# Kernel optimization log

Measured on AMD Instinct MI355X. Metric: run time of the kernel, lower is better.

Reference implementation:

```python
import jax, jax.numpy as jnp
import numpy as np
from jax import lax

B, L, F = 32, 2048, 76   # batch, seq_len, feat_dim
H = 128                  # conv hidden channels
D = 128                  # prototype dim (last 1x1 conv)
P = 128                  # number of prototypes
CLASS_SIZE = 2


def setup_inputs() -> dict:
    key = jax.random.key(0)
    ks = jax.random.split(key, 8)
    w = lambda k, shape: jax.random.normal(k, shape, jnp.float32) * 0.05
    return {
        "x": jax.random.normal(ks[0], (B, L, F), jnp.float32),
        "W1": w(ks[1], (H, F, 5)), "b1": jnp.zeros((H,), jnp.float32),
        "W2": w(ks[2], (H, H, 5)), "b2": jnp.zeros((H,), jnp.float32),
        "W3": w(ks[3], (H, H, 5)), "b3": jnp.zeros((H,), jnp.float32),
        "Wo1": w(ks[4], (D, H)), "bo1": jnp.zeros((D,), jnp.float32),
        "Wo2": w(ks[5], (D, D)), "bo2": jnp.zeros((D,), jnp.float32),
        "prototypes": jax.random.uniform(ks[6], (P, D), jnp.float32),
        "protop_classes": jnp.concatenate([jnp.zeros(P // 2, jnp.int32), jnp.ones(P // 2, jnp.int32)]),
    }


def _conv1d_same(h, W, b):
    # h: (B, C, L), W: (O, C, K=5), symmetric padding 2 == torch padding=k//2
    y = lax.conv_general_dilated(h, W, window_strides=(1,), padding=[(2, 2)],
                                 dimension_numbers=("NCW", "OIW", "NCW"))
    return y + b[None, :, None]


def _maxpool2(h):
    return lax.reduce_window(h, -jnp.inf, lax.max, (1, 1, 2), (1, 1, 2), "VALID")


def reference(x, W1, b1, W2, b2, W3, b3, Wo1, bo1, Wo2, bo2, prototypes, protop_classes):
    h = jnp.transpose(x, (0, 2, 1))  # (B, F, L)
    for W, b in ((W1, b1), (W2, b2), (W3, b3)):
        h = _maxpool2(jax.nn.relu(_conv1d_same(h, W, b)))
    # 1x1 convs as channel matmuls
    h = jax.nn.relu(jnp.einsum("bcl,oc->bol", h, Wo1) + bo1[None, :, None])
    h = jax.nn.relu(jnp.einsum("bcl,oc->bol", h, Wo2) + bo2[None, :, None])
    f = jnp.transpose(h, (0, 2, 1))  # (B, Lp=256, D)
    # l2_conv via ||a-b||^2 = ||a||^2 - 2 a.b + ||b||^2 (same math, GEMM form)
    d2 = (jnp.sum(f * f, axis=-1, keepdims=True)
          - 2.0 * jnp.einsum("bld,pd->blp", f, prototypes)
          + jnp.sum(prototypes * prototypes, axis=-1))  # (B, Lp, P)
    dis = jnp.sqrt(jnp.maximum(d2, 1e-12))
    min_dis = jnp.min(dis, axis=1)  # (B, P): min over patches
    # dis2sim, 'log' activation
    sim = jnp.log((min_dis + 1.0) / (min_dis + 1e-4))
    # init_weights: last_layer.weight[i,j] = 1 if protop_classes[j]==i else -0.5
    lw = jnp.where(protop_classes[None, :] == jnp.arange(CLASS_SIZE)[:, None], 1.0, -0.5)
    out = jax.nn.sigmoid(sim @ lw.T)  # (B, CLASS_SIZE)
    return out, min_dis
```

## Files before the change

kernel.cpp:

```cpp
#include <hip/hip_runtime.h>
#include <cmath>


typedef __attribute__((ext_vector_type(8))) short short8;
typedef __attribute__((ext_vector_type(4))) float f32x4;

__device__ __forceinline__ unsigned short f2bf(float v) {
    union { float f; unsigned u; } x; x.f = v;
    unsigned r = x.u + 0x7fffu + ((x.u >> 16) & 1u);
    return (unsigned short)(r >> 16);
}
__device__ __forceinline__ float bf2f(unsigned short b) {
    union { unsigned u; float f; } x; x.u = ((unsigned)b) << 16;
    return x.f;
}

__device__ void pack_conv_w(int t, int total, const float* __restrict__ W, int C,
                            unsigned short* __restrict__ dst)
{
    if (t >= total) return;
    int lane = t & 63, rest = t >> 6;
    int mf = rest & 7; rest >>= 3;
    int kk = rest % 5, cc = rest / 5;
    int m = mf * 16 + (lane & 15);
    int cb = cc * 32 + (lane >> 4) * 8;
    unsigned short v[8];
#pragma unroll
    for (int j = 0; j < 8; ++j) {
        int c = cb + j;
        v[j] = (c < C) ? f2bf(W[((size_t)m * C + c) * 5 + kk]) : (unsigned short)0;
    }
    *(uint4*)&dst[(size_t)t * 8] = *(uint4*)v;
}

__device__ void pack_mat(int t, const float* __restrict__ M, unsigned short* __restrict__ dst)
{
    if (t >= 2048) return;
    int lane = t & 63, mf = (t >> 6) & 7, cc = t >> 9;
    int m = mf * 16 + (lane & 15);
    int c0 = cc * 32 + (lane >> 4) * 8;
    unsigned short v[8];
#pragma unroll
    for (int j = 0; j < 8; ++j) v[j] = f2bf(M[(size_t)m * 128 + c0 + j]);
    *(uint4*)&dst[(size_t)t * 8] = *(uint4*)v;
}

__global__ __launch_bounds__(256)
void prep_weights_kernel(const float* __restrict__ W1, const float* __restrict__ W2,
                         const float* __restrict__ W3, const float* __restrict__ Wo1,
                         const float* __restrict__ Wo2, const float* __restrict__ protos,
                         unsigned short* A1, unsigned short* A2, unsigned short* A3,
                         unsigned short* AW1, unsigned short* AW2, unsigned short* AP,
                         float* pn, unsigned* pm_bits)
{
    int t = blockIdx.x * 256 + threadIdx.x;
    switch (blockIdx.y) {
    case 0: pack_conv_w(t, 7680,  W1, 76,  A1); break;
    case 1: pack_conv_w(t, 10240, W2, 128, A2); break;
    case 2: pack_conv_w(t, 10240, W3, 128, A3); break;
    case 3: pack_mat(t, Wo1, AW1); break;
    case 4: pack_mat(t, Wo2, AW2); break;
    case 5: pack_mat(t, protos, AP); break;
    case 6:
        if (t < 128) {
            float s = 0.f;
            for (int d = 0; d < 128; ++d) {
                float v = bf2f(f2bf(protos[(size_t)t * 128 + d]));
                s = fmaf(v, v, s);
            }
            pn[t] = s;
        }
        break;
    case 7:
        if (t < 4096) pm_bits[t] = 0x7F800000u;
        break;
    }
}

__global__ __launch_bounds__(256)
void conv1_mfma(const float* __restrict__ x, const unsigned short* __restrict__ Af,
                const float* __restrict__ bias, unsigned short* __restrict__ out)
{
    constexpr int LIN = 2048, LOUT = 1024, CPL = 104;
    __shared__ __align__(16) unsigned short s_in[68 * CPL];
    __shared__ float s_bias[128];

    const int tid = threadIdx.x;
    const int b   = blockIdx.y;
    const int l0  = blockIdx.x * 64;

    if (tid < 128) s_bias[tid] = bias[tid];

    for (int idx = tid; idx < 68 * 24; idx += 256) {
        int pos = idx / 24, c0 = (idx % 24) * 4;
        int l = l0 - 2 + pos;
        unsigned short v[4] = {0, 0, 0, 0};
        if (c0 < 76 && l >= 0 && l < LIN) {
            float4 xv = *(const float4*)&x[((size_t)b * LIN + l) * 76 + c0];
            v[0] = f2bf(xv.x); v[1] = f2bf(xv.y); v[2] = f2bf(xv.z); v[3] = f2bf(xv.w);
        }
        *(uint2*)&s_in[pos * CPL + c0] = *(uint2*)v;
    }
    __syncthreads();

    const int lane = tid & 63;
    const int mf0  = (tid >> 6) * 2;
    const int lc   = lane & 15;
    const int lk   = (lane >> 4) * 8;

    const f32x4 zero = {0.f, 0.f, 0.f, 0.f};
    f32x4 acc[2][4];
#pragma unroll
    for (int i = 0; i < 2; ++i)
#pragma unroll
        for (int j = 0; j < 4; ++j) acc[i][j] = zero;

    for (int cc = 0; cc < 3; ++cc) {
#pragma unroll
        for (int kk = 0; kk < 5; ++kk) {
            const int step = cc * 5 + kk;
            short8 a[2];
#pragma unroll
            for (int i = 0; i < 2; ++i)
                a[i] = *(const short8*)&Af[(((size_t)step * 8 + mf0 + i) * 64 + lane) * 8];
            short8 bb[4];
#pragma unroll
            for (int j = 0; j < 4; ++j)
                bb[j] = *(const short8*)&s_in[(j * 16 + lc + kk) * CPL + cc * 32 + lk];
#pragma unroll
            for (int i = 0; i < 2; ++i)
#pragma unroll
                for (int j = 0; j < 4; ++j)
                    acc[i][j] = __builtin_amdgcn_mfma_f32_16x16x32_bf16(a[i], bb[j], acc[i][j], 0, 0, 0);
        }
    }

    const int lp0 = l0 >> 1;
#pragma unroll
    for (int i = 0; i < 2; ++i) {
        const int ch0 = (mf0 + i) * 16 + (lane >> 4) * 4;
#pragma unroll
        for (int j = 0; j < 4; ++j) {
            const int n = j * 16 + lc;
            unsigned short pk[4];
#pragma unroll
            for (int r = 0; r < 4; ++r) {
                float v = fmaxf(acc[i][j][r] + s_bias[ch0 + r], 0.f);
                float o = __shfl_xor(v, 1);
                pk[r] = f2bf(fmaxf(v, o));
            }
            if ((lc & 1) == 0)
                *(uint2*)&out[((size_t)b * LOUT + lp0 + (n >> 1)) * 128 + ch0] = *(uint2*)pk;
        }
    }
}

__global__ __launch_bounds__(256)
void conv2_mfma(const unsigned short* __restrict__ in, const unsigned short* __restrict__ Af,
                const float* __restrict__ bias, unsigned short* __restrict__ out)
{
    constexpr int LIN = 1024, LOUT = 512, CPL = 136;
    __shared__ __align__(16) unsigned short s_in[68 * CPL];
    __shared__ float s_bias[128];

    const int tid = threadIdx.x;
    const int b   = blockIdx.y;
    const int l0  = blockIdx.x * 64;

    if (tid < 128) s_bias[tid] = bias[tid];

    for (int idx = tid; idx < 68 * 16; idx += 256) {
        int pos = idx >> 4, co = (idx & 15) * 8;
        int l = l0 - 2 + pos;
        uint4 v = make_uint4(0u, 0u, 0u, 0u);
        if (l >= 0 && l < LIN)
            v = *(const uint4*)&in[((size_t)b * LIN + l) * 128 + co];
        *(uint4*)&s_in[pos * CPL + co] = v;
    }
    __syncthreads();

    const int lane = tid & 63;
    const int mf0  = (tid >> 6) * 2;
    const int lc   = lane & 15;
    const int lk   = (lane >> 4) * 8;

    const f32x4 zero = {0.f, 0.f, 0.f, 0.f};
    f32x4 acc[2][4];
#pragma unroll
    for (int i = 0; i < 2; ++i)
#pragma unroll
        for (int j = 0; j < 4; ++j) acc[i][j] = zero;

    for (int cc = 0; cc < 4; ++cc) {
#pragma unroll
        for (int kk = 0; kk < 5; ++kk) {
            const int step = cc * 5 + kk;
            short8 a[2];
#pragma unroll
            for (int i = 0; i < 2; ++i)
                a[i] = *(const short8*)&Af[(((size_t)step * 8 + mf0 + i) * 64 + lane) * 8];
            short8 bb[4];
#pragma unroll
            for (int j = 0; j < 4; ++j)
                bb[j] = *(const short8*)&s_in[(j * 16 + lc + kk) * CPL + cc * 32 + lk];
#pragma unroll
            for (int i = 0; i < 2; ++i)
#pragma unroll
                for (int j = 0; j < 4; ++j)
                    acc[i][j] = __builtin_amdgcn_mfma_f32_16x16x32_bf16(a[i], bb[j], acc[i][j], 0, 0, 0);
        }
    }

    const int lp0 = l0 >> 1;
#pragma unroll
    for (int i = 0; i < 2; ++i) {
        const int ch0 = (mf0 + i) * 16 + (lane >> 4) * 4;
#pragma unroll
        for (int j = 0; j < 4; ++j) {
            const int n = j * 16 + lc;
            unsigned short pk[4];
#pragma unroll
            for (int r = 0; r < 4; ++r) {
                float v = fmaxf(acc[i][j][r] + s_bias[ch0 + r], 0.f);
                float o = __shfl_xor(v, 1);
                pk[r] = f2bf(fmaxf(v, o));
            }
            if ((lc & 1) == 0)
                *(uint2*)&out[((size_t)b * LOUT + lp0 + (n >> 1)) * 128 + ch0] = *(uint2*)pk;
        }
    }
}

__global__ __launch_bounds__(256)
void conv3_head(const unsigned short* __restrict__ in, const unsigned short* __restrict__ Af,
                const float* __restrict__ bias,
                const unsigned short* __restrict__ AW1, const float* __restrict__ bo1,
                const unsigned short* __restrict__ AW2, const float* __restrict__ bo2,
                const unsigned short* __restrict__ AP,  const float* __restrict__ pn,
                unsigned* __restrict__ pm_bits)
{
    constexpr int LIN = 512, CPL = 136, CP = 136;
    __shared__ __align__(16) unsigned short s_in[68 * CPL];
    __shared__ __align__(16) unsigned short s_f[32 * CP];
    __shared__ float s_bias[128];
    __shared__ float s_part[4 * 32];
    __shared__ float s_fn[32];

    const int tid = threadIdx.x;
    const int b   = blockIdx.y;
    const int l0  = blockIdx.x * 64;

    if (tid < 128) s_bias[tid] = bias[tid];

    for (int idx = tid; idx < 68 * 16; idx += 256) {
        int pos = idx >> 4, co = (idx & 15) * 8;
        int l = l0 - 2 + pos;
        uint4 v = make_uint4(0u, 0u, 0u, 0u);
        if (l >= 0 && l < LIN)
            v = *(const uint4*)&in[((size_t)b * LIN + l) * 128 + co];
        *(uint4*)&s_in[pos * CPL + co] = v;
    }
    __syncthreads();

    const int lane = tid & 63;
    const int mf0  = (tid >> 6) * 2;
    const int lc   = lane & 15;
    const int lk   = (lane >> 4) * 8;

    const f32x4 zero = {0.f, 0.f, 0.f, 0.f};

    f32x4 acc[2][4];
#pragma unroll
    for (int i = 0; i < 2; ++i)
#pragma unroll
        for (int j = 0; j < 4; ++j) acc[i][j] = zero;

    for (int cc = 0; cc < 4; ++cc) {
#pragma unroll
        for (int kk = 0; kk < 5; ++kk) {
            const int step = cc * 5 + kk;
            short8 a[2];
#pragma unroll
            for (int i = 0; i < 2; ++i)
                a[i] = *(const short8*)&Af[(((size_t)step * 8 + mf0 + i) * 64 + lane) * 8];
            short8 bb[4];
#pragma unroll
            for (int j = 0; j < 4; ++j)
                bb[j] = *(const short8*)&s_in[(j * 16 + lc + kk) * CPL + cc * 32 + lk];
#pragma unroll
            for (int i = 0; i < 2; ++i)
#pragma unroll
                for (int j = 0; j < 4; ++j)
                    acc[i][j] = __builtin_amdgcn_mfma_f32_16x16x32_bf16(a[i], bb[j], acc[i][j], 0, 0, 0);
        }
    }

#pragma unroll
    for (int i = 0; i < 2; ++i) {
        const int ch0 = (mf0 + i) * 16 + (lane >> 4) * 4;
#pragma unroll
        for (int j = 0; j < 4; ++j) {
            const int n = j * 16 + lc;
            unsigned short pk[4];
#pragma unroll
            for (int r = 0; r < 4; ++r) {
                float v = fmaxf(acc[i][j][r] + s_bias[ch0 + r], 0.f);
                float o = __shfl_xor(v, 1);
                pk[r] = f2bf(fmaxf(v, o));
            }
            if ((lc & 1) == 0)
                *(uint2*)&s_f[(n >> 1) * CP + ch0] = *(uint2*)pk;
        }
    }
    __syncthreads();

    f32x4 hacc[2][2];

    auto gemm32 = [&](const unsigned short* __restrict__ A) {
#pragma unroll
        for (int i = 0; i < 2; ++i)
#pragma unroll
            for (int j = 0; j < 2; ++j) hacc[i][j] = zero;
        for (int cc = 0; cc < 4; ++cc) {
            short8 a[2];
#pragma unroll
            for (int i = 0; i < 2; ++i)
                a[i] = *(const short8*)&A[(((size_t)cc * 8 + mf0 + i) * 64 + lane) * 8];
            short8 bb[2];
#pragma unroll
            for (int j = 0; j < 2; ++j)
                bb[j] = *(const short8*)&s_f[(j * 16 + lc) * CP + cc * 32 + lk];
#pragma unroll
            for (int i = 0; i < 2; ++i)
#pragma unroll
                for (int j = 0; j < 2; ++j)
                    hacc[i][j] = __builtin_amdgcn_mfma_f32_16x16x32_bf16(a[i], bb[j], hacc[i][j], 0, 0, 0);
        }
    };

    auto store_relu32 = [&](const float* __restrict__ bv) {
        __syncthreads();
#pragma unroll
        for (int i = 0; i < 2; ++i) {
            const int ch0 = (mf0 + i) * 16 + (lane >> 4) * 4;
#pragma unroll
            for (int j = 0; j < 2; ++j) {
                const int n = j * 16 + lc;
                unsigned short pk[4];
#pragma unroll
                for (int r = 0; r < 4; ++r)
                    pk[r] = f2bf(fmaxf(hacc[i][j][r] + bv[ch0 + r], 0.f));
                *(uint2*)&s_f[n * CP + ch0] = *(uint2*)pk;
            }
        }
        __syncthreads();
    };

    gemm32(AW1); store_relu32(bo1);
    gemm32(AW2); store_relu32(bo2);

    if (tid < 128) {
        int n = tid >> 2, part = tid & 3;
        float s = 0.f;
        for (int c = part * 32; c < part * 32 + 32; ++c) {
            float v = bf2f(s_f[n * CP + c]);
            s = fmaf(v, v, s);
        }
        s_part[part * 32 + n] = s;
    }
    __syncthreads();
    if (tid < 32)
        s_fn[tid] = s_part[tid] + s_part[32 + tid] + s_part[64 + tid] + s_part[96 + tid];
    __syncthreads();

    gemm32(AP);

#pragma unroll
    for (int i = 0; i < 2; ++i) {
#pragma unroll
        for (int r = 0; r < 4; ++r) {
            const int p = (mf0 + i) * 16 + (lane >> 4) * 4 + r;
            float m = 3.0e38f;
#pragma unroll
            for (int j = 0; j < 2; ++j) {
                const int n = j * 16 + lc;
                float d2 = s_fn[n] + pn[p] - 2.f * hacc[i][j][r];
                m = fminf(m, sqrtf(fmaxf(d2, 1e-12f)));
            }
#pragma unroll
            for (int s = 1; s < 16; s <<= 1)
                m = fminf(m, __shfl_xor(m, s));
            if (lc == 0)
                atomicMin(&pm_bits[(size_t)b * 128 + p], __float_as_uint(m));
        }
    }
}

__global__ __launch_bounds__(128)
void finalize_kernel(const float* __restrict__ pm,
                     const int* __restrict__ classes,
                     float* __restrict__ out)
{
    __shared__ float r0[128], r1[128];
    const int b = blockIdx.x, p = threadIdx.x;
    float m = pm[(size_t)b * 128 + p];
    out[64 + b * 128 + p] = m;

    float sim = logf((m + 1.0f) / (m + 1e-4f));
    int cls = classes[p];
    r0[p] = (cls == 0) ? sim : -0.5f * sim;
    r1[p] = (cls == 1) ? sim : -0.5f * sim;
    __syncthreads();
    for (int s = 64; s > 0; s >>= 1) {
        if (p < s) { r0[p] += r0[p + s]; r1[p] += r1[p + s]; }
        __syncthreads();
    }
    if (p == 0) {
        out[b * 2 + 0] = 1.f / (1.f + expf(-r0[0]));
        out[b * 2 + 1] = 1.f / (1.f + expf(-r1[0]));
    }
}

extern "C" void kernel_launch(void* const* d_in, const int* in_sizes, int n_in,
                              void* d_out, int out_size, void* d_ws, size_t ws_size,
                              hipStream_t stream)
{
    (void)in_sizes; (void)n_in; (void)out_size; (void)ws_size;
    const float* x    = (const float*)d_in[0];
    const float* W1   = (const float*)d_in[1];
    const float* b1   = (const float*)d_in[2];
    const float* W2   = (const float*)d_in[3];
    const float* b2   = (const float*)d_in[4];
    const float* W3   = (const float*)d_in[5];
    const float* b3   = (const float*)d_in[6];
    const float* Wo1  = (const float*)d_in[7];
    const float* bo1  = (const float*)d_in[8];
    const float* Wo2  = (const float*)d_in[9];
    const float* bo2  = (const float*)d_in[10];
    const float* prot = (const float*)d_in[11];
    const int*   cls  = (const int*)d_in[12];
    float* out = (float*)d_out;

    char* ws = (char*)d_ws;
    unsigned short* h1 = (unsigned short*)(ws);
    unsigned short* h2 = (unsigned short*)(ws + 8388608);
    const size_t FR = 12582912;
    unsigned short* A1  = (unsigned short*)(ws + FR);
    unsigned short* A2  = (unsigned short*)(ws + FR + 122880);
    unsigned short* A3  = (unsigned short*)(ws + FR + 286720);
    unsigned short* AW1 = (unsigned short*)(ws + FR + 450560);
    unsigned short* AW2 = (unsigned short*)(ws + FR + 483328);
    unsigned short* AP  = (unsigned short*)(ws + FR + 516096);
    float*          pn  = (float*)(ws + FR + 548864);
    unsigned*       pm  = (unsigned*)(ws + FR + 549376);

    prep_weights_kernel<<<dim3(40, 8), 256, 0, stream>>>(W1, W2, W3, Wo1, Wo2, prot,
                                                         A1, A2, A3, AW1, AW2, AP, pn, pm);
    conv1_mfma<<<dim3(32, 32), 256, 0, stream>>>(x,  A1, b1, h1);
    conv2_mfma<<<dim3(16, 32), 256, 0, stream>>>(h1, A2, b2, h2);
    conv3_head<<<dim3(8, 32), 256, 0, stream>>>(h2, A3, b3, AW1, bo1, AW2, bo2, AP, pn, pm);
    finalize_kernel<<<32, 128, 0, stream>>>((const float*)pm, cls, out);
}
```

Before: 133.1 us.

## Fuse all three conv stages and head into one kernel with halo recompute

Replaces the separate conv1, conv2 and conv3+head kernels with one 512-thread kernel per (batch, 256-position tile). Each block loads an input tile with an 18-position halo, runs conv1 into shared memory, then conv2 and conv3 from shared memory, and finishes with the 1x1 head and prototype distances. This removes the global-memory round trips of the h1/h2 intermediates and two kernel launches. In exchange it recomputes halo columns, launches only 256 blocks, and needs large shared memory and many accumulator registers, which may limit occupancy.

```diff
diff --git a/kernel.cpp b/kernel.cpp
--- a/kernel.cpp
+++ b/kernel.cpp
@@ -77,45 +77,20 @@
     }
 }
 
-__global__ __launch_bounds__(256)
-void conv1_mfma(const float* __restrict__ x, const unsigned short* __restrict__ Af,
-                const float* __restrict__ bias, unsigned short* __restrict__ out)
-{
-    constexpr int LIN = 2048, LOUT = 1024, CPL = 104;
-    __shared__ __align__(16) unsigned short s_in[68 * CPL];
-    __shared__ float s_bias[128];
-
-    const int tid = threadIdx.x;
-    const int b   = blockIdx.y;
-    const int l0  = blockIdx.x * 64;
-
-    if (tid < 128) s_bias[tid] = bias[tid];
-
-    for (int idx = tid; idx < 68 * 24; idx += 256) {
-        int pos = idx / 24, c0 = (idx % 24) * 4;
-        int l = l0 - 2 + pos;
-        unsigned short v[4] = {0, 0, 0, 0};
-        if (c0 < 76 && l >= 0 && l < LIN) {
-            float4 xv = *(const float4*)&x[((size_t)b * LIN + l) * 76 + c0];
-            v[0] = f2bf(xv.x); v[1] = f2bf(xv.y); v[2] = f2bf(xv.z); v[3] = f2bf(xv.w);
-        }
-        *(uint2*)&s_in[pos * CPL + c0] = *(uint2*)v;
-    }
-    __syncthreads();
-
-    const int lane = tid & 63;
-    const int mf0  = (tid >> 6) * 2;
-    const int lc   = lane & 15;
-    const int lk   = (lane >> 4) * 8;
-
-    const f32x4 zero = {0.f, 0.f, 0.f, 0.f};
-    f32x4 acc[2][4];
+template <int NJ, int NCC, int STRIDE, int ROWOFF, int ROWMAX>
+__device__ __forceinline__ void conv_k(const unsigned short* __restrict__ Af,
+                                       const unsigned short* __restrict__ sIn,
+                                       int nbase, int mf0, int lane,
+                                       f32x4 (&acc)[2][NJ])
+{
+    const int lc = lane & 15;
+    const int lk = (lane >> 4) * 8;
 #pragma unroll
     for (int i = 0; i < 2; ++i)
 #pragma unroll
-        for (int j = 0; j < 4; ++j) acc[i][j] = zero;
-
-    for (int cc = 0; cc < 3; ++cc) {
+        for (int j = 0; j < NJ; ++j) acc[i][j] = (f32x4){0.f, 0.f, 0.f, 0.f};
+
+    for (int cc = 0; cc < NCC; ++cc) {
 #pragma unroll
         for (int kk = 0; kk < 5; ++kk) {
             const int step = cc * 5 + kk;
@@ -123,247 +98,208 @@
 #pragma unroll
             for (int i = 0; i < 2; ++i)
                 a[i] = *(const short8*)&Af[(((size_t)step * 8 + mf0 + i) * 64 + lane) * 8];
-            short8 bb[4];
-#pragma unroll
-            for (int j = 0; j < 4; ++j)
-                bb[j] = *(const short8*)&s_in[(j * 16 + lc + kk) * CPL + cc * 32 + lk];
-#pragma unroll
-            for (int i = 0; i < 2; ++i)
-#pragma unroll
-                for (int j = 0; j < 4; ++j)
+            short8 bb[NJ];
+#pragma unroll
+            for (int j = 0; j < NJ; ++j) {
+                int row = nbase + j * 16 + lc + kk + ROWOFF;
+                if (ROWMAX >= 0) row = min(max(row, 0), ROWMAX);
+                bb[j] = *(const short8*)&sIn[row * STRIDE + cc * 32 + lk];
+            }
+#pragma unroll
+            for (int j = 0; j < NJ; ++j)
+#pragma unroll
+                for (int i = 0; i < 2; ++i)
                     acc[i][j] = __builtin_amdgcn_mfma_f32_16x16x32_bf16(a[i], bb[j], acc[i][j], 0, 0, 0);
         }
     }
-
-    const int lp0 = l0 >> 1;
+}
+
+__device__ __forceinline__ void gemm_head(const unsigned short* __restrict__ Af,
+                                          const unsigned short* __restrict__ s_f,
+                                          int nbase, int mf0, int lane,
+                                          f32x4 (&acc)[2])
+{
+    const int lc = lane & 15;
+    const int lk = (lane >> 4) * 8;
+    acc[0] = (f32x4){0.f, 0.f, 0.f, 0.f};
+    acc[1] = (f32x4){0.f, 0.f, 0.f, 0.f};
+#pragma unroll
+    for (int cc = 0; cc < 4; ++cc) {
+        short8 a[2];
+#pragma unroll
+        for (int i = 0; i < 2; ++i)
+            a[i] = *(const short8*)&Af[(((size_t)cc * 8 + mf0 + i) * 64 + lane) * 8];
+        short8 bb = *(const short8*)&s_f[(nbase + lc) * 136 + cc * 32 + lk];
+#pragma unroll
+        for (int i = 0; i < 2; ++i)
+            acc[i] = __builtin_amdgcn_mfma_f32_16x16x32_bf16(a[i], bb, acc[i], 0, 0, 0);
+    }
+}
+
+__global__ __launch_bounds__(512, 2)
+void mega_kernel(const float* __restrict__ x,
+                 const unsigned short* __restrict__ A1, const float* __restrict__ b1,
+                 const unsigned short* __restrict__ A2, const float* __restrict__ b2,
+                 const unsigned short* __restrict__ A3, const float* __restrict__ b3,
+                 const unsigned short* __restrict__ AW1, const float* __restrict__ bo1,
+                 const unsigned short* __restrict__ AW2, const float* __restrict__ bo2,
+                 const unsigned short* __restrict__ AP,  const float* __restrict__ pn,
+                 unsigned* __restrict__ pm_bits)
+{
+    __shared__ __align__(16) unsigned short s_x[324 * 104];
+    __shared__ __align__(16) unsigned short s_h1[140 * 136];
+    __shared__ float s_cb[768];
+    __shared__ float s_part[128];
+    __shared__ float s_fn[32];
+    unsigned short* s_h2 = s_x;
+    unsigned short* s_f  = s_x + 9248;
+
+    const int tid  = threadIdx.x;
+    const int q    = blockIdx.x;
+    const int b    = blockIdx.y;
+    const int lane = tid & 63;
+    const int wid  = tid >> 6;
+    const int mf0  = (wid & 3) * 2;
+    const int ng   = wid >> 2;
+    const int lc   = lane & 15;
+    const int lq   = (lane >> 4) * 4;
+
+    for (int i = tid; i < 768; i += 512) {
+        const float* src = (i < 128) ? b1 : (i < 256) ? b2 : (i < 384) ? b3
+                         : (i < 512) ? bo1 : (i < 640) ? bo2 : pn;
+        s_cb[i] = src[i & 127];
+    }
+
+    const int xbase = 256 * q - 18;
+    for (int idx = tid; idx < 324 * 24; idx += 512) {
+        int pos = idx / 24, c0 = (idx % 24) * 4;
+        int l = xbase + pos;
+        unsigned short v[4] = {0, 0, 0, 0};
+        if (c0 < 76 && l >= 0 && l < 2048) {
+            float4 xv = *(const float4*)&x[((size_t)b * 2048 + l) * 76 + c0];
+            v[0] = f2bf(xv.x); v[1] = f2bf(xv.y); v[2] = f2bf(xv.z); v[3] = f2bf(xv.w);
+        }
+        *(uint2*)&s_x[pos * 104 + c0] = *(uint2*)v;
+    }
+    __syncthreads();
+
+    {
+        f32x4 acc[2][10];
+        conv_k<10, 3, 104, 0, -1>(A1, s_x, ng * 160, mf0, lane, acc);
+
+#pragma unroll
+        for (int i = 0; i < 2; ++i) {
+            const int ch0 = (mf0 + i) * 16 + lq;
+#pragma unroll
+            for (int j = 0; j < 10; ++j) {
+                const int nl = ng * 160 + j * 16 + lc;
+                unsigned short pk[4];
+#pragma unroll
+                for (int r = 0; r < 4; ++r) {
+                    float v = fmaxf(acc[i][j][r] + s_cb[ch0 + r], 0.f);
+                    float o = __shfl_xor(v, 1);
+                    pk[r] = f2bf(fmaxf(v, o));
+                }
+                if ((lc & 1) == 0) {
+                    int jh = (nl >> 1) - 2;
+                    int jg = 128 * q - 6 + jh;
+                    if (jh >= 0 && jh < 140) {
+                        uint2 val = (jg >= 0 && jg < 1024) ? *(uint2*)pk : make_uint2(0u, 0u);
+                        *(uint2*)&s_h1[jh * 136 + ch0] = val;
+                    }
+                }
+            }
+        }
+    }
+    __syncthreads();
+
+    {
+        f32x4 acc[2][6];
+        conv_k<6, 4, 136, -4, 139>(A2, s_h1, ng * 96, mf0, lane, acc);
+
+#pragma unroll
+        for (int i = 0; i < 2; ++i) {
+            const int ch0 = (mf0 + i) * 16 + lq;
+#pragma unroll
+            for (int j = 0; j < 6; ++j) {
+                const int nl = ng * 96 + j * 16 + lc;
+                unsigned short pk[4];
+#pragma unroll
+                for (int r = 0; r < 4; ++r) {
+                    float v = fmaxf(acc[i][j][r] + s_cb[128 + ch0 + r], 0.f);
+                    float o = __shfl_xor(v, 1);
+                    pk[r] = f2bf(fmaxf(v, o));
+                }
+                if ((lc & 1) == 0) {
+                    int jh = (nl >> 1) - 2;
+                    int jg = 64 * q - 2 + jh;
+                    if (jh >= 0 && jh < 68) {
+                        uint2 val = (jg >= 0 && jg < 512) ? *(uint2*)pk : make_uint2(0u, 0u);
+                        *(uint2*)&s_h2[jh * 136 + ch0] = val;
+                    }
+                }
+            }
+        }
+    }
+    __syncthreads();
+
+    {
+        f32x4 acc[2][2];
+        conv_k<2, 4, 136, 0, -1>(A3, s_h2, ng * 32, mf0, lane, acc);
+
+#pragma unroll
+        for (int i = 0; i < 2; ++i) {
+            const int ch0 = (mf0 + i) * 16 + lq;
+#pragma unroll
+            for (int j = 0; j < 2; ++j) {
+                const int nl = ng * 32 + j * 16 + lc;
+                unsigned short pk[4];
+#pragma unroll
+                for (int r = 0; r < 4; ++r) {
+                    float v = fmaxf(acc[i][j][r] + s_cb[256 + ch0 + r], 0.f);
+                    float o = __shfl_xor(v, 1);
+                    pk[r] = f2bf(fmaxf(v, o));
+                }
+                if ((lc & 1) == 0)
+                    *(uint2*)&s_f[(nl >> 1) * 136 + ch0] = *(uint2*)pk;
+            }
+        }
+    }
+    __syncthreads();
+
+    f32x4 hacc[2];
+
+    gemm_head(AW1, s_f, ng * 16, mf0, lane, hacc);
+    __syncthreads();
 #pragma unroll
     for (int i = 0; i < 2; ++i) {
-        const int ch0 = (mf0 + i) * 16 + (lane >> 4) * 4;
-#pragma unroll
-        for (int j = 0; j < 4; ++j) {
-            const int n = j * 16 + lc;
-            unsigned short pk[4];
-#pragma unroll
-            for (int r = 0; r < 4; ++r) {
-                float v = fmaxf(acc[i][j][r] + s_bias[ch0 + r], 0.f);
-                float o = __shfl_xor(v, 1);
-                pk[r] = f2bf(fmaxf(v, o));
-            }
-            if ((lc & 1) == 0)
-                *(uint2*)&out[((size_t)b * LOUT + lp0 + (n >> 1)) * 128 + ch0] = *(uint2*)pk;
-        }
-    }
-}
-
-__global__ __launch_bounds__(256)
-void conv2_mfma(const unsigned short* __restrict__ in, const unsigned short* __restrict__ Af,
-                const float* __restrict__ bias, unsigned short* __restrict__ out)
-{
-    constexpr int LIN = 1024, LOUT = 512, CPL = 136;
-    __shared__ __align__(16) unsigned short s_in[68 * CPL];
-    __shared__ float s_bias[128];
-
-    const int tid = threadIdx.x;
-    const int b   = blockIdx.y;
-    const int l0  = blockIdx.x * 64;
-
-    if (tid < 128) s_bias[tid] = bias[tid];
-
-    for (int idx = tid; idx < 68 * 16; idx += 256) {
-        int pos = idx >> 4, co = (idx & 15) * 8;
-        int l = l0 - 2 + pos;
-        uint4 v = make_uint4(0u, 0u, 0u, 0u);
-        if (l >= 0 && l < LIN)
-            v = *(const uint4*)&in[((size_t)b * LIN + l) * 128 + co];
-        *(uint4*)&s_in[pos * CPL + co] = v;
-    }
-    __syncthreads();
-
-    const int lane = tid & 63;
-    const int mf0  = (tid >> 6) * 2;
-    const int lc   = lane & 15;
-    const int lk   = (lane >> 4) * 8;
-
-    const f32x4 zero = {0.f, 0.f, 0.f, 0.f};
-    f32x4 acc[2][4];
-#pragma unroll
-    for (int i = 0; i < 2; ++i)
-#pragma unroll
-        for (int j = 0; j < 4; ++j) acc[i][j] = zero;
-
-    for (int cc = 0; cc < 4; ++cc) {
-#pragma unroll
-        for (int kk = 0; kk < 5; ++kk) {
-            const int step = cc * 5 + kk;
-            short8 a[2];
-#pragma unroll
-            for (int i = 0; i < 2; ++i)
-                a[i] = *(const short8*)&Af[(((size_t)step * 8 + mf0 + i) * 64 + lane) * 8];
-            short8 bb[4];
-#pragma unroll
-            for (int j = 0; j < 4; ++j)
-                bb[j] = *(const short8*)&s_in[(j * 16 + lc + kk) * CPL + cc * 32 + lk];
-#pragma unroll
-            for (int i = 0; i < 2; ++i)
-#pragma unroll
-                for (int j = 0; j < 4; ++j)
-                    acc[i][j] = __builtin_amdgcn_mfma_f32_16x16x32_bf16(a[i], bb[j], acc[i][j], 0, 0, 0);
-        }
-    }
-
-    const int lp0 = l0 >> 1;
+        const int ch0 = (mf0 + i) * 16 + lq;
+        unsigned short pk[4];
+#pragma unroll
+        for (int r = 0; r < 4; ++r)
+            pk[r] = f2bf(fmaxf(hacc[i][r] + s_cb[384 + ch0 + r], 0.f));
+        *(uint2*)&s_f[(ng * 16 + lc) * 136 + ch0] = *(uint2*)pk;
+    }
+    __syncthreads();
+
+    gemm_head(AW2, s_f, ng * 16, mf0, lane, hacc);
+    __syncthreads();
 #pragma unroll
     for (int i = 0; i < 2; ++i) {
-        const int ch0 = (mf0 + i) * 16 + (lane >> 4) * 4;
-#pragma unroll
-        for (int j = 0; j < 4; ++j) {
-            const int n = j * 16 + lc;
-            unsigned short pk[4];
-#pragma unroll
-            for (int r = 0; r < 4; ++r) {
-                float v = fmaxf(acc[i][j][r] + s_bias[ch0 + r], 0.f);
-                float o = __shfl_xor(v, 1);
-                pk[r] = f2bf(fmaxf(v, o));
-            }
-            if ((lc & 1) == 0)
-                *(uint2*)&out[((size_t)b * LOUT + lp0 + (n >> 1)) * 128 + ch0] = *(uint2*)pk;
-        }
-    }
-}
-
-__global__ __launch_bounds__(256)
-void conv3_head(const unsigned short* __restrict__ in, const unsigned short* __restrict__ Af,
-                const float* __restrict__ bias,
-                const unsigned short* __restrict__ AW1, const float* __restrict__ bo1,
-                const unsigned short* __restrict__ AW2, const float* __restrict__ bo2,
-                const unsigned short* __restrict__ AP,  const float* __restrict__ pn,
-                unsigned* __restrict__ pm_bits)
-{
-    constexpr int LIN = 512, CPL = 136, CP = 136;
-    __shared__ __align__(16) unsigned short s_in[68 * CPL];
-    __shared__ __align__(16) unsigned short s_f[32 * CP];
-    __shared__ float s_bias[128];
-    __shared__ float s_part[4 * 32];
-    __shared__ float s_fn[32];
-
-    const int tid = threadIdx.x;
-    const int b   = blockIdx.y;
-    const int l0  = blockIdx.x * 64;
-
-    if (tid < 128) s_bias[tid] = bias[tid];
-
-    for (int idx = tid; idx < 68 * 16; idx += 256) {
-        int pos = idx >> 4, co = (idx & 15) * 8;
-        int l = l0 - 2 + pos;
-        uint4 v = make_uint4(0u, 0u, 0u, 0u);
-        if (l >= 0 && l < LIN)
-            v = *(const uint4*)&in[((size_t)b * LIN + l) * 128 + co];
-        *(uint4*)&s_in[pos * CPL + co] = v;
-    }
-    __syncthreads();
-
-    const int lane = tid & 63;
-    const int mf0  = (tid >> 6) * 2;
-    const int lc   = lane & 15;
-    const int lk   = (lane >> 4) * 8;
-
-    const f32x4 zero = {0.f, 0.f, 0.f, 0.f};
-
-    f32x4 acc[2][4];
-#pragma unroll
-    for (int i = 0; i < 2; ++i)
-#pragma unroll
-        for (int j = 0; j < 4; ++j) acc[i][j] = zero;
-
-    for (int cc = 0; cc < 4; ++cc) {
-#pragma unroll
-        for (int kk = 0; kk < 5; ++kk) {
-            const int step = cc * 5 + kk;
-            short8 a[2];
-#pragma unroll
-            for (int i = 0; i < 2; ++i)
-                a[i] = *(const short8*)&Af[(((size_t)step * 8 + mf0 + i) * 64 + lane) * 8];
-            short8 bb[4];
-#pragma unroll
-            for (int j = 0; j < 4; ++j)
-                bb[j] = *(const short8*)&s_in[(j * 16 + lc + kk) * CPL + cc * 32 + lk];
-#pragma unroll
-            for (int i = 0; i < 2; ++i)
-#pragma unroll
-                for (int j = 0; j < 4; ++j)
-                    acc[i][j] = __builtin_amdgcn_mfma_f32_16x16x32_bf16(a[i], bb[j], acc[i][j], 0, 0, 0);
-        }
-    }
-
-#pragma unroll
-    for (int i = 0; i < 2; ++i) {
-        const int ch0 = (mf0 + i) * 16 + (lane >> 4) * 4;
-#pragma unroll
-        for (int j = 0; j < 4; ++j) {
-            const int n = j * 16 + lc;
-            unsigned short pk[4];
-#pragma unroll
-            for (int r = 0; r < 4; ++r) {
-                float v = fmaxf(acc[i][j][r] + s_bias[ch0 + r], 0.f);
-                float o = __shfl_xor(v, 1);
-                pk[r] = f2bf(fmaxf(v, o));
-            }
-            if ((lc & 1) == 0)
-                *(uint2*)&s_f[(n >> 1) * CP + ch0] = *(uint2*)pk;
-        }
-    }
-    __syncthreads();
-
-    f32x4 hacc[2][2];
-
-    auto gemm32 = [&](const unsigned short* __restrict__ A) {
-#pragma unroll
-        for (int i = 0; i < 2; ++i)
-#pragma unroll
-            for (int j = 0; j < 2; ++j) hacc[i][j] = zero;
-        for (int cc = 0; cc < 4; ++cc) {
-            short8 a[2];
-#pragma unroll
-            for (int i = 0; i < 2; ++i)
-                a[i] = *(const short8*)&A[(((size_t)cc * 8 + mf0 + i) * 64 + lane) * 8];
-            short8 bb[2];
-#pragma unroll
-            for (int j = 0; j < 2; ++j)
-                bb[j] = *(const short8*)&s_f[(j * 16 + lc) * CP + cc * 32 + lk];
-#pragma unroll
-            for (int i = 0; i < 2; ++i)
-#pragma unroll
-                for (int j = 0; j < 2; ++j)
-                    hacc[i][j] = __builtin_amdgcn_mfma_f32_16x16x32_bf16(a[i], bb[j], hacc[i][j], 0, 0, 0);
-        }
-    };
-
-    auto store_relu32 = [&](const float* __restrict__ bv) {
-        __syncthreads();
-#pragma unroll
-        for (int i = 0; i < 2; ++i) {
-            const int ch0 = (mf0 + i) * 16 + (lane >> 4) * 4;
-#pragma unroll
-            for (int j = 0; j < 2; ++j) {
-                const int n = j * 16 + lc;
-                unsigned short pk[4];
-#pragma unroll
-                for (int r = 0; r < 4; ++r)
-                    pk[r] = f2bf(fmaxf(hacc[i][j][r] + bv[ch0 + r], 0.f));
-                *(uint2*)&s_f[n * CP + ch0] = *(uint2*)pk;
-            }
-        }
-        __syncthreads();
-    };
-
-    gemm32(AW1); store_relu32(bo1);
-    gemm32(AW2); store_relu32(bo2);
+        const int ch0 = (mf0 + i) * 16 + lq;
+        unsigned short pk[4];
+#pragma unroll
+        for (int r = 0; r < 4; ++r)
+            pk[r] = f2bf(fmaxf(hacc[i][r] + s_cb[512 + ch0 + r], 0.f));
+        *(uint2*)&s_f[(ng * 16 + lc) * 136 + ch0] = *(uint2*)pk;
+    }
+    __syncthreads();
 
     if (tid < 128) {
         int n = tid >> 2, part = tid & 3;
         float s = 0.f;
         for (int c = part * 32; c < part * 32 + 32; ++c) {
-            float v = bf2f(s_f[n * CP + c]);
+            float v = bf2f(s_f[n * 136 + c]);
             s = fmaf(v, v, s);
         }
         s_part[part * 32 + n] = s;
@@ -373,20 +309,15 @@
         s_fn[tid] = s_part[tid] + s_part[32 + tid] + s_part[64 + tid] + s_part[96 + tid];
     __syncthreads();
 
-    gemm32(AP);
-
+    gemm_head(AP, s_f, ng * 16, mf0, lane, hacc);
 #pragma unroll
     for (int i = 0; i < 2; ++i) {
 #pragma unroll
         for (int r = 0; r < 4; ++r) {
-            const int p = (mf0 + i) * 16 + (lane >> 4) * 4 + r;
-            float m = 3.0e38f;
-#pragma unroll
-            for (int j = 0; j < 2; ++j) {
-                const int n = j * 16 + lc;
-                float d2 = s_fn[n] + pn[p] - 2.f * hacc[i][j][r];
-                m = fminf(m, sqrtf(fmaxf(d2, 1e-12f)));
-            }
+            const int p = (mf0 + i) * 16 + lq + r;
+            const int n = ng * 16 + lc;
+            float d2 = s_fn[n] + s_cb[640 + p] - 2.f * hacc[i][r];
+            float m = sqrtf(fmaxf(d2, 1e-12f));
 #pragma unroll
             for (int s = 1; s < 16; s <<= 1)
                 m = fminf(m, __shfl_xor(m, s));
@@ -442,22 +373,18 @@
     float* out = (float*)d_out;
 
     char* ws = (char*)d_ws;
-    unsigned short* h1 = (unsigned short*)(ws);
-    unsigned short* h2 = (unsigned short*)(ws + 8388608);
-    const size_t FR = 12582912;
-    unsigned short* A1  = (unsigned short*)(ws + FR);
-    unsigned short* A2  = (unsigned short*)(ws + FR + 122880);
-    unsigned short* A3  = (unsigned short*)(ws + FR + 286720);
-    unsigned short* AW1 = (unsigned short*)(ws + FR + 450560);
-    unsigned short* AW2 = (unsigned short*)(ws + FR + 483328);
-    unsigned short* AP  = (unsigned short*)(ws + FR + 516096);
-    float*          pn  = (float*)(ws + FR + 548864);
-    unsigned*       pm  = (unsigned*)(ws + FR + 549376);
+    unsigned short* A1  = (unsigned short*)(ws);
+    unsigned short* A2  = (unsigned short*)(ws + 122880);
+    unsigned short* A3  = (unsigned short*)(ws + 286720);
+    unsigned short* AW1 = (unsigned short*)(ws + 450560);
+    unsigned short* AW2 = (unsigned short*)(ws + 483328);
+    unsigned short* AP  = (unsigned short*)(ws + 516096);
+    float*          pn  = (float*)(ws + 548864);
+    unsigned*       pm  = (unsigned*)(ws + 549376);
 
     prep_weights_kernel<<<dim3(40, 8), 256, 0, stream>>>(W1, W2, W3, Wo1, Wo2, prot,
                                                          A1, A2, A3, AW1, AW2, AP, pn, pm);
-    conv1_mfma<<<dim3(32, 32), 256, 0, stream>>>(x,  A1, b1, h1);
-    conv2_mfma<<<dim3(16, 32), 256, 0, stream>>>(h1, A2, b2, h2);
-    conv3_head<<<dim3(8, 32), 256, 0, stream>>>(h2, A3, b3, AW1, bo1, AW2, bo2, AP, pn, pm);
+    mega_kernel<<<dim3(8, 32), 512, 0, stream>>>(x, A1, b1, A2, b2, A3, b3,
+                                                 AW1, bo1, AW2, bo2, AP, pn, pm);
     finalize_kernel<<<32, 128, 0, stream>>>((const float*)pm, cls, out);
 }
```

Result: faster. 130.4 us (-2.1%).
